# Performance work log

Measured on AMD Instinct MI355X. Metric: run time of the kernel, lower is better.

Reference implementation:

```python
import jax, jax.numpy as jnp
import numpy as np

K = 16          # self.nn_size
BALL2 = 0.2     # ball_size * 2, compared against squared L2 dists (faiss convention)

def _knn(q, db, k):
    # squared L2 pairwise distances (B,N,M) via ||q||^2 + ||db||^2 - 2 q.db
    d2 = (jnp.sum(q * q, -1)[..., None]
          + jnp.sum(db * db, -1)[..., None, :]
          - 2.0 * jnp.einsum('bnc,bmc->bnm', q, db))
    neg_d, idx = jax.lax.top_k(-d2, k)   # k smallest distances
    return -neg_d, idx                    # (B,N,K), (B,N,K)

def _cond_numbers(grouped, nball, B, N, C):
    # center by masked-ball mean, then singular values of (K,C) groups
    center = jnp.sum(grouped, axis=2, keepdims=True) / nball[..., None]
    centered = (grouped - center).reshape(-1, K, C)
    S = jnp.linalg.svd(centered, compute_uv=False)   # descending, (B*N, min(K,C))
    return (S[:, 0] / (S[:, -1] + S[:, 0])).reshape(B, N)

def setup_inputs() -> dict:
    key = jax.random.key(0)
    k1, k2 = jax.random.split(key)
    ref_points = jax.random.uniform(k1, (2, 8192, 3), dtype=jnp.float32)
    points = jax.random.uniform(k2, (2, 8192, 3), dtype=jnp.float32)
    return {"ref_points": ref_points, "points": points}

def reference(ref_points, points):
    B, N, C = ref_points.shape
    dist, idx = _knn(ref_points, ref_points, K)
    mask = dist < BALL2                                  # (B,N,K)
    nball = jnp.sum(mask.astype(ref_points.dtype), -1, keepdims=True)  # (B,N,1)

    gather = jax.vmap(lambda p, i: p[i])                 # (N,C),(N,K)->(N,K,C)
    grouped_ref = gather(ref_points, idx)                # (B,N,K,C)
    grouped_ref = jnp.where(mask[..., None], grouped_ref, 0.0)  # masked_fill_ (in-place, kept)
    ref_cond = _cond_numbers(grouped_ref, nball, B, N, C)

    grouped = gather(points, idx)                        # (B,N,K,C)
    # NOTE: original calls masked_fill (non-inplace) and DISCARDS the result -> no masking here
    cond = _cond_numbers(grouped, nball, B, N, C)

    # metric: MSE with mean reduction
    return jnp.mean((cond - ref_cond) ** 2)
```

## Files before the change

### kernel.cpp

```cpp
#include <hip/hip_runtime.h>

#define NPTS   8192
#define KNN    16
#define G      10
#define NCELLS 1000
#define CELLSZ 0.1f
#define BALL2f 0.2f
#define TRUNCM 0xFFFFE000u
#define IDXM   0x1FFFu
#define NBLK   256
#define FLTMAX 3.402823466e+38f

#define WS_ACC    0
#define WS_DONE   8
#define WS_STARTS 16
#define WS_RSORT  8032

__device__ __forceinline__ int clampg(int v) { return v < 0 ? 0 : (v > G - 1 ? G - 1 : v); }

__global__ __launch_bounds__(1024) void prep_kernel(
        const float* __restrict__ ref, int* __restrict__ gstarts,
        float4* __restrict__ rs, double* __restrict__ acc, int* __restrict__ done) {
    __shared__ int cnt[NCELLS];
    __shared__ int ssum[NCELLS + 1];
    __shared__ int wsum[16];
    const int b = blockIdx.x, t = threadIdx.x;
    const int w = t >> 6, lane = t & 63;
    if (b == 0 && t == 0) { acc[0] = 0.0; done[0] = 0; }
    if (t < NCELLS) cnt[t] = 0;
    __syncthreads();

    const float4* rb4 = reinterpret_cast<const float4*>(ref + (size_t)b * NPTS * 3) + t * 6;
    float4 A = rb4[0], B = rb4[1], C = rb4[2], D = rb4[3], E = rb4[4], F = rb4[5];
    float xs[8] = {A.x, A.w, B.z, C.y, D.x, D.w, E.z, F.y};
    float ys[8] = {A.y, B.x, B.w, C.z, D.y, E.x, E.w, F.z};
    float zs[8] = {A.z, B.y, C.x, C.w, D.z, E.y, F.x, F.w};
    int cells[8], slots[8];
    #pragma unroll
    for (int k = 0; k < 8; ++k) {
        int c = (clampg((int)(zs[k] * (float)G)) * G + clampg((int)(ys[k] * (float)G))) * G
              + clampg((int)(xs[k] * (float)G));
        cells[k] = c;
        slots[k] = atomicAdd(&cnt[c], 1);
    }
    __syncthreads();

    int v = (t < NCELLS) ? cnt[t] : 0;
    #pragma unroll
    for (int off = 1; off < 64; off <<= 1) {
        int u = __shfl_up(v, off, 64);
        if (lane >= off) v += u;
    }
    if (lane == 63) wsum[w] = v;
    __syncthreads();
    if (t == 0) {
        int run = 0;
        for (int i2 = 0; i2 < 16; ++i2) { int tv = wsum[i2]; wsum[i2] = run; run += tv; }
    }
    __syncthreads();
    if (t < NCELLS) ssum[t + 1] = v + wsum[w];
    if (t == 0) ssum[0] = 0;
    __syncthreads();
    if (t <= NCELLS) gstarts[b * (NCELLS + 1) + t] = ssum[t];

    #pragma unroll
    for (int k = 0; k < 8; ++k) {
        int pos = ssum[cells[k]] + slots[k];
        rs[(size_t)b * NPTS + pos] = make_float4(xs[k], ys[k], zs[k],
                                                 __uint_as_float((unsigned)(t * 8 + k)));
    }
}

__device__ __noinline__ double cond3(double xx, double xy, double xz,
                                     double yy, double yz, double zz) {
    double q  = (xx + yy + zz) * (1.0 / 3.0);
    double a  = xx - q, b = yy - q, c = zz - q;
    double p1 = xy * xy + xz * xz + yz * yz;
    double p2 = a * a + b * b + c * c + 2.0 * p1;
    if (p2 <= 0.0) return 0.5;
    double p   = sqrt(p2 * (1.0 / 6.0));
    double inv = 1.0 / p;
    double b00 = a * inv, b11 = b * inv, b22 = c * inv;
    double b01 = xy * inv, b02 = xz * inv, b12 = yz * inv;
    double detB = b00 * (b11 * b22 - b12 * b12)
                - b01 * (b01 * b22 - b12 * b02)
                + b02 * (b01 * b12 - b11 * b02);
    double r = 0.5 * detB;
    r = fmin(1.0, fmax(-1.0, r));
    double phi = acos(r) * (1.0 / 3.0);
    double l0 = q + 2.0 * p * cos(phi);
    double l2 = q + 2.0 * p * cos(phi + 2.0943951023931953);
    double s0 = sqrt(fmax(l0, 0.0));
    double s2 = sqrt(fmax(l2, 0.0));
    return s0 / (s0 + s2);
}

__global__ __launch_bounds__(1024) void cond_knn_kernel(
        const float* __restrict__ ref, const float* __restrict__ pts,
        const float4* __restrict__ rs, const int* __restrict__ gstarts,
        double* __restrict__ acc, int* __restrict__ done,
        float* __restrict__ out) {
    __shared__ unsigned sld[8][64][17];
    __shared__ int ss[NCELLS + 1];
    __shared__ unsigned cutp[64];
    __shared__ unsigned char doneA[64];
    __shared__ int flagS;

    const int tid  = threadIdx.x;
    const int w    = tid >> 6;
    const int lane = tid & 63;
    const int b     = blockIdx.x >> 7;
    const int qbase = (blockIdx.x & 127) << 6;
    const float4* rs4 = rs + (size_t)b * NPTS;

    for (int i = tid; i < NCELLS + 1; i += 1024)
        ss[i] = gstarts[b * (NCELLS + 1) + i];
    __syncthreads();

    float4 Q = rs4[qbase + lane];
    const float qx = Q.x, qy = Q.y, qz = Q.z;
    const int cx = clampg((int)(qx * (float)G));
    const int cy = clampg((int)(qy * (float)G));
    const int cz = clampg((int)(qz * (float)G));

    unsigned bq[KNN];
    #pragma unroll
    for (int k = 0; k < KNN; ++k) bq[k] = 0xFFFFFFFFu;

    auto ins1 = [&](unsigned vk, unsigned cutv) {
        unsigned cv = cutv < bq[15] ? cutv : bq[15];
        if (vk < cv) {
            bq[15] = vk;
            #pragma unroll
            for (int kk = 15; kk >= 1; --kk) {
                unsigned l2 = min(bq[kk - 1], bq[kk]);
                unsigned h2 = max(bq[kk - 1], bq[kk]);
                bq[kk - 1] = l2; bq[kk] = h2;
            }
        }
    };

    auto scanRange = [&](int s0, int s1, unsigned cutv) {
        int t2 = s0;
        for (; t2 + 4 <= s1; t2 += 4) {
            float4 P0 = rs4[t2 + 0];
            float4 P1 = rs4[t2 + 1];
            float4 P2 = rs4[t2 + 2];
            float4 P3 = rs4[t2 + 3];
            float dx0 = qx - P0.x, dy0 = qy - P0.y, dz0 = qz - P0.z;
            float dx1 = qx - P1.x, dy1 = qy - P1.y, dz1 = qz - P1.z;
            float dx2 = qx - P2.x, dy2 = qy - P2.y, dz2 = qz - P2.z;
            float dx3 = qx - P3.x, dy3 = qy - P3.y, dz3 = qz - P3.z;
            float d0 = fmaf(dx0, dx0, fmaf(dy0, dy0, dz0 * dz0));
            float d1 = fmaf(dx1, dx1, fmaf(dy1, dy1, dz1 * dz1));
            float d2 = fmaf(dx2, dx2, fmaf(dy2, dy2, dz2 * dz2));
            float d3 = fmaf(dx3, dx3, fmaf(dy3, dy3, dz3 * dz3));
            unsigned k0 = (__float_as_uint(d0) & TRUNCM) | __float_as_uint(P0.w);
            unsigned k1 = (__float_as_uint(d1) & TRUNCM) | __float_as_uint(P1.w);
            unsigned k2 = (__float_as_uint(d2) & TRUNCM) | __float_as_uint(P2.w);
            unsigned k3 = (__float_as_uint(d3) & TRUNCM) | __float_as_uint(P3.w);
            unsigned mn = min(min(k0, k1), min(k2, k3));
            unsigned cv = cutv < bq[15] ? cutv : bq[15];
            if (mn < cv) {
                ins1(k0, cutv); ins1(k1, cutv); ins1(k2, cutv); ins1(k3, cutv);
            }
        }
        for (; t2 < s1; ++t2) {
            float4 P = rs4[t2];
            float dx = qx - P.x, dy = qy - P.y, dz = qz - P.z;
            float d = fmaf(dx, dx, fmaf(dy, dy, dz * dz));
            ins1((__float_as_uint(d) & TRUNCM) | __float_as_uint(P.w), cutv);
        }
    };

    for (int it = w; it < 36; it += 16) {
        int q   = it & 3;
        int row = it >> 2;
        int dz = row / 3 - 1;
        int dy = row % 3 - 1;
        int ny = cy + dy, nz = cz + dz;
        if ((unsigned)ny > (unsigned)(G - 1) || (unsigned)nz > (unsigned)(G - 1)) continue;
        int x0 = cx - 1 < 0 ? 0 : cx - 1;
        int x1 = cx + 1 > G - 1 ? G - 1 : cx + 1;
        int c0 = (nz * G + ny) * G + x0;
        int s0 = ss[c0];
        int s1 = ss[c0 + (x1 - x0) + 1];
        int len = s1 - s0;
        int qs = s0 + ((len * q) >> 2);
        int qe = s0 + ((len * (q + 1)) >> 2);
        scanRange(qs, qe, 0xFFFFFFFFu);
    }

    for (int r = 2;; ++r) {
        #pragma unroll
        for (int rnd = 0; rnd < 4; ++rnd) {
            int s = 1 << rnd;
            int slot = w >> (rnd + 1);
            __syncthreads();
            if ((w & (2 * s - 1)) == s) {
                #pragma unroll
                for (int k = 0; k < KNN; ++k) sld[slot][lane][k] = bq[k];
            }
            __syncthreads();
            if ((w & (2 * s - 1)) == 0) {
                unsigned t[KNN];
                #pragma unroll
                for (int i = 0; i < KNN; ++i) t[i] = min(bq[i], sld[slot][lane][KNN - 1 - i]);
                #pragma unroll
                for (int s2 = 8; s2 >= 1; s2 >>= 1) {
                    #pragma unroll
                    for (int i = 0; i < KNN; ++i) {
                        if ((i & s2) == 0) {
                            unsigned l2 = min(t[i], t[i | s2]);
                            unsigned h2 = max(t[i], t[i | s2]);
                            t[i] = l2; t[i | s2] = h2;
                        }
                    }
                }
                #pragma unroll
                for (int k = 0; k < KNN; ++k) bq[k] = t[k];
            }
        }

        if (tid == 0) flagS = 0;
        __syncthreads();
        if (w == 0) {
            int rd = r - 1;
            float mx = FLTMAX;
            if (cx - rd > 0)     mx = fminf(mx, qx - (float)(cx - rd) * CELLSZ);
            if (cx + rd < G - 1) mx = fminf(mx, (float)(cx + rd + 1) * CELLSZ - qx);
            if (cy - rd > 0)     mx = fminf(mx, qy - (float)(cy - rd) * CELLSZ);
            if (cy + rd < G - 1) mx = fminf(mx, (float)(cy + rd + 1) * CELLSZ - qy);
            if (cz - rd > 0)     mx = fminf(mx, qz - (float)(cz - rd) * CELLSZ);
            if (cz + rd < G - 1) mx = fminf(mx, (float)(cz + rd + 1) * CELLSZ - qz);
            float d16t = __uint_as_float(bq[15] & TRUNCM);
            bool dn = d16t <= mx * mx * 0.998f;
            cutp[lane]  = bq[15];
            doneA[lane] = dn ? 1 : 0;
            if (__any(!dn) && lane == 0) flagS = 1;
        }
        __syncthreads();
        if (!flagS || r > G) break;

        if (w != 0) {
            #pragma unroll
            for (int k = 0; k < KNN; ++k) bq[k] = 0xFFFFFFFFu;
        }
        unsigned cut = cutp[lane];
        float cutub = __uint_as_float(cut | IDXM);
        bool active = !doneA[lane];
        int cc = 0;
        for (int dz = -r; dz <= r; ++dz)
        for (int dy = -r; dy <= r; ++dy)
        for (int dx = -r; dx <= r; ++dx) {
            int adx = dx < 0 ? -dx : dx, ady = dy < 0 ? -dy : dy, adz = dz < 0 ? -dz : dz;
            int m = adx > ady ? adx : ady; m = m > adz ? m : adz;
            if (m != r) continue;
            int myc = cc++;
            if ((myc & 15) != w) continue;
            if (!active) continue;
            int nx = cx + dx, ny = cy + dy, nz = cz + dz;
            if ((unsigned)nx > (unsigned)(G - 1) || (unsigned)ny > (unsigned)(G - 1) ||
                (unsigned)nz > (unsigned)(G - 1)) continue;
            float ex0 = (float)nx * CELLSZ;
            float ey0 = (float)ny * CELLSZ;
            float ez0 = (float)nz * CELLSZ;
            float ddx = fmaxf(0.f, fmaxf(ex0 - qx, qx - ex0 - CELLSZ));
            float ddy = fmaxf(0.f, fmaxf(ey0 - qy, qy - ey0 - CELLSZ));
            float ddz = fmaxf(0.f, fmaxf(ez0 - qz, qz - ez0 - CELLSZ));
            float d2min = fmaf(ddx, ddx, fmaf(ddy, ddy, ddz * ddz));
            if (d2min > cutub) continue;
            int cell = (nz * G + ny) * G + nx;
            scanRange(ss[cell], ss[cell + 1], cut);
        }
    }

    if (w != 0) return;

    const float* refb = ref + (size_t)b * NPTS * 3;
    const float* ptsb = pts + (size_t)b * NPTS * 3;
    float rx[KNN], ry[KNN], rz[KNN], px[KNN], py[KNN], pz[KNN];
    int mbits = 0;
    float sRx = 0.f, sRy = 0.f, sRz = 0.f, sPx = 0.f, sPy = 0.f, sPz = 0.f;
    #pragma unroll
    for (int k = 0; k < KNN; ++k) {
        int i = (int)(bq[k] & IDXM);
        float du = __uint_as_float(bq[k] & TRUNCM);
        rx[k] = refb[3 * i]; ry[k] = refb[3 * i + 1]; rz[k] = refb[3 * i + 2];
        px[k] = ptsb[3 * i]; py[k] = ptsb[3 * i + 1]; pz[k] = ptsb[3 * i + 2];
        if (du < BALL2f) {
            mbits |= (1 << k);
            sRx += rx[k]; sRy += ry[k]; sRz += rz[k];
        }
        sPx += px[k]; sPy += py[k]; sPz += pz[k];
    }
    int nb = __popc(mbits);
    double inb = 1.0 / (double)nb;
    double cRx = (double)sRx * inb, cRy = (double)sRy * inb, cRz = (double)sRz * inb;
    double cPx = (double)sPx * inb, cPy = (double)sPy * inb, cPz = (double)sPz * inb;

    double Rxx = 0, Rxy = 0, Rxz = 0, Ryy = 0, Ryz = 0, Rzz = 0;
    double Pxx = 0, Pxy = 0, Pxz = 0, Pyy = 0, Pyz = 0, Pzz = 0;
    #pragma unroll
    for (int k = 0; k < KNN; ++k) {
        bool m = (mbits >> k) & 1;
        double ax = (m ? (double)rx[k] : 0.0) - cRx;
        double ay = (m ? (double)ry[k] : 0.0) - cRy;
        double az = (m ? (double)rz[k] : 0.0) - cRz;
        Rxx += ax * ax; Rxy += ax * ay; Rxz += ax * az;
        Ryy += ay * ay; Ryz += ay * az; Rzz += az * az;
        double bx = (double)px[k] - cPx;
        double by = (double)py[k] - cPy;
        double bz = (double)pz[k] - cPz;
        Pxx += bx * bx; Pxy += bx * by; Pxz += bx * bz;
        Pyy += by * by; Pyz += by * bz; Pzz += bz * bz;
    }
    double condR = cond3(Rxx, Rxy, Rxz, Ryy, Ryz, Rzz);
    double condP = cond3(Pxx, Pxy, Pxz, Pyy, Pyz, Pzz);
    double t = condP - condR;
    t = t * t;

    #pragma unroll
    for (int off = 32; off > 0; off >>= 1) t += __shfl_down(t, off);
    if (lane == 0) {
        atomicAdd(acc, t);
        __threadfence();
        int prev = atomicAdd(done, 1);
        if (prev == NBLK - 1) {
            __threadfence();
            double total = atomicAdd(acc, 0.0);
            out[0] = (float)(total * (1.0 / 16384.0));
        }
    }
}

extern "C" void kernel_launch(void* const* d_in, const int* in_sizes, int n_in,
                              void* d_out, int out_size, void* d_ws, size_t ws_size,
                              hipStream_t stream) {
    const float* ref = (const float*)d_in[0];
    const float* pts = (const float*)d_in[1];
    char* ws = (char*)d_ws;
    double* acc   = (double*)(ws + WS_ACC);
    int* done     = (int*)(ws + WS_DONE);
    int* gstarts  = (int*)(ws + WS_STARTS);
    float4* rsort = (float4*)(ws + WS_RSORT);

    hipLaunchKernelGGL(prep_kernel,     dim3(2),    dim3(1024), 0, stream,
                       ref, gstarts, rsort, acc, done);
    hipLaunchKernelGGL(cond_knn_kernel, dim3(NBLK), dim3(1024), 0, stream,
                       ref, pts, rsort, gstarts, acc, done, (float*)d_out);
}
```

Measured before the change: 94.77 us.

## Use one wavefront per query block instead of sixteen cooperating waves

Each 64-query block now runs on a single wavefront that scans every neighbouring cell itself. This drops the shared-memory bitonic merges of per-wave top-16 lists, the block-wide barriers and the shared cut/done flags between search rings. The cost is less parallelism: 256 blocks of 64 threads put far fewer waves on the GPU, and each lane's serial scan grows about sixteenfold. Latency may therefore rise unless the removed sync and merge overhead was dominant.

```diff
diff --git a/kernel.cpp b/kernel.cpp
--- a/kernel.cpp
+++ b/kernel.cpp
@@ -95,25 +95,20 @@
     return s0 / (s0 + s2);
 }
 
-__global__ __launch_bounds__(1024) void cond_knn_kernel(
+__global__ __launch_bounds__(64) void cond_knn_kernel(
         const float* __restrict__ ref, const float* __restrict__ pts,
         const float4* __restrict__ rs, const int* __restrict__ gstarts,
         double* __restrict__ acc, int* __restrict__ done,
         float* __restrict__ out) {
-    __shared__ unsigned sld[8][64][17];
     __shared__ int ss[NCELLS + 1];
-    __shared__ unsigned cutp[64];
-    __shared__ unsigned char doneA[64];
-    __shared__ int flagS;
-
-    const int tid  = threadIdx.x;
-    const int w    = tid >> 6;
-    const int lane = tid & 63;
-    const int b     = blockIdx.x >> 7;
-    const int qbase = (blockIdx.x & 127) << 6;
+
+    const int lane = threadIdx.x;
+    const int blk  = blockIdx.x;
+    const int b     = blk >> 7;
+    const int qbase = (blk & 127) << 6;
     const float4* rs4 = rs + (size_t)b * NPTS;
 
-    for (int i = tid; i < NCELLS + 1; i += 1024)
+    for (int i = lane; i < NCELLS + 1; i += 64)
         ss[i] = gstarts[b * (NCELLS + 1) + i];
     __syncthreads();
 
@@ -127,9 +122,8 @@
     #pragma unroll
     for (int k = 0; k < KNN; ++k) bq[k] = 0xFFFFFFFFu;
 
-    auto ins1 = [&](unsigned vk, unsigned cutv) {
-        unsigned cv = cutv < bq[15] ? cutv : bq[15];
-        if (vk < cv) {
+    auto ins1 = [&](unsigned vk) {
+        if (vk < bq[15]) {
             bq[15] = vk;
             #pragma unroll
             for (int kk = 15; kk >= 1; --kk) {
@@ -140,7 +134,7 @@
         }
     };
 
-    auto scanRange = [&](int s0, int s1, unsigned cutv) {
+    auto scanRange = [&](int s0, int s1) {
         int t2 = s0;
         for (; t2 + 4 <= s1; t2 += 4) {
             float4 P0 = rs4[t2 + 0];
@@ -160,104 +154,58 @@
             unsigned k2 = (__float_as_uint(d2) & TRUNCM) | __float_as_uint(P2.w);
             unsigned k3 = (__float_as_uint(d3) & TRUNCM) | __float_as_uint(P3.w);
             unsigned mn = min(min(k0, k1), min(k2, k3));
-            unsigned cv = cutv < bq[15] ? cutv : bq[15];
-            if (mn < cv) {
-                ins1(k0, cutv); ins1(k1, cutv); ins1(k2, cutv); ins1(k3, cutv);
-            }
+            if (mn < bq[15]) { ins1(k0); ins1(k1); ins1(k2); ins1(k3); }
         }
         for (; t2 < s1; ++t2) {
             float4 P = rs4[t2];
             float dx = qx - P.x, dy = qy - P.y, dz = qz - P.z;
             float d = fmaf(dx, dx, fmaf(dy, dy, dz * dz));
-            ins1((__float_as_uint(d) & TRUNCM) | __float_as_uint(P.w), cutv);
+            ins1((__float_as_uint(d) & TRUNCM) | __float_as_uint(P.w));
         }
     };
 
-    for (int it = w; it < 36; it += 16) {
-        int q   = it & 3;
-        int row = it >> 2;
+    #pragma unroll 1
+    for (int row = 0; row < 9; ++row) {
         int dz = row / 3 - 1;
         int dy = row % 3 - 1;
         int ny = cy + dy, nz = cz + dz;
-        if ((unsigned)ny > (unsigned)(G - 1) || (unsigned)nz > (unsigned)(G - 1)) continue;
+        bool ok = (unsigned)ny <= (unsigned)(G - 1) && (unsigned)nz <= (unsigned)(G - 1);
         int x0 = cx - 1 < 0 ? 0 : cx - 1;
         int x1 = cx + 1 > G - 1 ? G - 1 : cx + 1;
         int c0 = (nz * G + ny) * G + x0;
-        int s0 = ss[c0];
-        int s1 = ss[c0 + (x1 - x0) + 1];
-        int len = s1 - s0;
-        int qs = s0 + ((len * q) >> 2);
-        int qe = s0 + ((len * (q + 1)) >> 2);
-        scanRange(qs, qe, 0xFFFFFFFFu);
-    }
-
-    for (int r = 2;; ++r) {
-        #pragma unroll
-        for (int rnd = 0; rnd < 4; ++rnd) {
-            int s = 1 << rnd;
-            int slot = w >> (rnd + 1);
-            __syncthreads();
-            if ((w & (2 * s - 1)) == s) {
-                #pragma unroll
-                for (int k = 0; k < KNN; ++k) sld[slot][lane][k] = bq[k];
-            }
-            __syncthreads();
-            if ((w & (2 * s - 1)) == 0) {
-                unsigned t[KNN];
-                #pragma unroll
-                for (int i = 0; i < KNN; ++i) t[i] = min(bq[i], sld[slot][lane][KNN - 1 - i]);
-                #pragma unroll
-                for (int s2 = 8; s2 >= 1; s2 >>= 1) {
-                    #pragma unroll
-                    for (int i = 0; i < KNN; ++i) {
-                        if ((i & s2) == 0) {
-                            unsigned l2 = min(t[i], t[i | s2]);
-                            unsigned h2 = max(t[i], t[i | s2]);
-                            t[i] = l2; t[i | s2] = h2;
-                        }
-                    }
-                }
-                #pragma unroll
-                for (int k = 0; k < KNN; ++k) bq[k] = t[k];
-            }
-        }
-
-        if (tid == 0) flagS = 0;
-        __syncthreads();
-        if (w == 0) {
-            int rd = r - 1;
-            float mx = FLTMAX;
-            if (cx - rd > 0)     mx = fminf(mx, qx - (float)(cx - rd) * CELLSZ);
-            if (cx + rd < G - 1) mx = fminf(mx, (float)(cx + rd + 1) * CELLSZ - qx);
-            if (cy - rd > 0)     mx = fminf(mx, qy - (float)(cy - rd) * CELLSZ);
-            if (cy + rd < G - 1) mx = fminf(mx, (float)(cy + rd + 1) * CELLSZ - qy);
-            if (cz - rd > 0)     mx = fminf(mx, qz - (float)(cz - rd) * CELLSZ);
-            if (cz + rd < G - 1) mx = fminf(mx, (float)(cz + rd + 1) * CELLSZ - qz);
-            float d16t = __uint_as_float(bq[15] & TRUNCM);
-            bool dn = d16t <= mx * mx * 0.998f;
-            cutp[lane]  = bq[15];
-            doneA[lane] = dn ? 1 : 0;
-            if (__any(!dn) && lane == 0) flagS = 1;
-        }
-        __syncthreads();
-        if (!flagS || r > G) break;
-
-        if (w != 0) {
-            #pragma unroll
-            for (int k = 0; k < KNN; ++k) bq[k] = 0xFFFFFFFFu;
-        }
-        unsigned cut = cutp[lane];
-        float cutub = __uint_as_float(cut | IDXM);
-        bool active = !doneA[lane];
-        int cc = 0;
+        int s0 = ok ? ss[c0] : 0;
+        int s1 = ok ? ss[c0 + (x1 - x0) + 1] : 0;
+        scanRange(s0, s1);
+    }
+
+    auto margin2 = [&](int rd) {
+        float mx = FLTMAX;
+        if (cx - rd > 0)     mx = fminf(mx, qx - (float)(cx - rd) * CELLSZ);
+        if (cx + rd < G - 1) mx = fminf(mx, (float)(cx + rd + 1) * CELLSZ - qx);
+        if (cy - rd > 0)     mx = fminf(mx, qy - (float)(cy - rd) * CELLSZ);
+        if (cy + rd < G - 1) mx = fminf(mx, (float)(cy + rd + 1) * CELLSZ - qy);
+        if (cz - rd > 0)     mx = fminf(mx, qz - (float)(cz - rd) * CELLSZ);
+        if (cz + rd < G - 1) mx = fminf(mx, (float)(cz + rd + 1) * CELLSZ - qz);
+        return mx * mx * 0.998f;
+    };
+
+    bool dn;
+    {
+        float d16t = __uint_as_float(bq[15] & TRUNCM);
+        dn = d16t <= margin2(1);
+    }
+    #pragma unroll 1
+    for (int r = 2; __any(!dn) && r <= G; ++r) {
+        bool active = !dn;
+        #pragma unroll 1
         for (int dz = -r; dz <= r; ++dz)
+        #pragma unroll 1
         for (int dy = -r; dy <= r; ++dy)
+        #pragma unroll 1
         for (int dx = -r; dx <= r; ++dx) {
             int adx = dx < 0 ? -dx : dx, ady = dy < 0 ? -dy : dy, adz = dz < 0 ? -dz : dz;
             int m = adx > ady ? adx : ady; m = m > adz ? m : adz;
             if (m != r) continue;
-            int myc = cc++;
-            if ((myc & 15) != w) continue;
             if (!active) continue;
             int nx = cx + dx, ny = cy + dy, nz = cz + dz;
             if ((unsigned)nx > (unsigned)(G - 1) || (unsigned)ny > (unsigned)(G - 1) ||
@@ -269,13 +217,14 @@
             float ddy = fmaxf(0.f, fmaxf(ey0 - qy, qy - ey0 - CELLSZ));
             float ddz = fmaxf(0.f, fmaxf(ez0 - qz, qz - ez0 - CELLSZ));
             float d2min = fmaf(ddx, ddx, fmaf(ddy, ddy, ddz * ddz));
+            float cutub = __uint_as_float(bq[15] | IDXM);
             if (d2min > cutub) continue;
             int cell = (nz * G + ny) * G + nx;
-            scanRange(ss[cell], ss[cell + 1], cut);
-        }
-    }
-
-    if (w != 0) return;
+            scanRange(ss[cell], ss[cell + 1]);
+        }
+        float d16t = __uint_as_float(bq[15] & TRUNCM);
+        dn = d16t <= margin2(r);
+    }
 
     const float* refb = ref + (size_t)b * NPTS * 3;
     const float* ptsb = pts + (size_t)b * NPTS * 3;
@@ -347,6 +296,6 @@
 
     hipLaunchKernelGGL(prep_kernel,     dim3(2),    dim3(1024), 0, stream,
                        ref, gstarts, rsort, acc, done);
-    hipLaunchKernelGGL(cond_knn_kernel, dim3(NBLK), dim3(1024), 0, stream,
+    hipLaunchKernelGGL(cond_knn_kernel, dim3(NBLK), dim3(64),   0, stream,
                        ref, pts, rsort, gstarts, acc, done, (float*)d_out);
 }
```

New measurement: 120.0 us. 26.7% more time.

## Split each query across two half-wavefronts and double block count

Applied to the files above, without the earlier changes.

Each block now handles 32 queries with 512 threads, and each query is processed by two lanes that scan disjoint halves of every cell range. The two partial top-16 lists are merged with a cross-half shuffle. This doubles the grid to 512 blocks so more of the GPU's compute units stay busy and per-lane scan length shrinks. The cost is an extra merge step and redundant work on the duplicated half-lanes during the epilogue.

```diff
diff --git a/kernel.cpp b/kernel.cpp
--- a/kernel.cpp
+++ b/kernel.cpp
@@ -8,7 +8,7 @@
 #define BALL2f 0.2f
 #define TRUNCM 0xFFFFE000u
 #define IDXM   0x1FFFu
-#define NBLK   256
+#define NBLK   512
 #define FLTMAX 3.402823466e+38f
 
 #define WS_ACC    0
@@ -95,29 +95,31 @@
     return s0 / (s0 + s2);
 }
 
-__global__ __launch_bounds__(1024) void cond_knn_kernel(
+__global__ __launch_bounds__(512, 4) void cond_knn_kernel(
         const float* __restrict__ ref, const float* __restrict__ pts,
         const float4* __restrict__ rs, const int* __restrict__ gstarts,
         double* __restrict__ acc, int* __restrict__ done,
         float* __restrict__ out) {
-    __shared__ unsigned sld[8][64][17];
     __shared__ int ss[NCELLS + 1];
-    __shared__ unsigned cutp[64];
-    __shared__ unsigned char doneA[64];
+    __shared__ unsigned sld[4][64][17];
+    __shared__ unsigned cutp[32];
+    __shared__ unsigned char doneA[32];
     __shared__ int flagS;
 
     const int tid  = threadIdx.x;
     const int w    = tid >> 6;
     const int lane = tid & 63;
-    const int b     = blockIdx.x >> 7;
-    const int qbase = (blockIdx.x & 127) << 6;
+    const int half = lane >> 5;
+    const int ql   = lane & 31;
+    const int b     = blockIdx.x >> 8;
+    const int qbase = (blockIdx.x & 255) << 5;
     const float4* rs4 = rs + (size_t)b * NPTS;
 
-    for (int i = tid; i < NCELLS + 1; i += 1024)
+    for (int i = tid; i < NCELLS + 1; i += 512)
         ss[i] = gstarts[b * (NCELLS + 1) + i];
     __syncthreads();
 
-    float4 Q = rs4[qbase + lane];
+    float4 Q = rs4[qbase + ql];
     const float qx = Q.x, qy = Q.y, qz = Q.z;
     const int cx = clampg((int)(qx * (float)G));
     const int cy = clampg((int)(qy * (float)G));
@@ -141,8 +143,11 @@
     };
 
     auto scanRange = [&](int s0, int s1, unsigned cutv) {
-        int t2 = s0;
-        for (; t2 + 4 <= s1; t2 += 4) {
+        int len = s1 - s0;
+        int a  = s0 + ((len * half) >> 1);
+        int e  = s0 + ((len * (half + 1)) >> 1);
+        int t2 = a;
+        for (; t2 + 4 <= e; t2 += 4) {
             float4 P0 = rs4[t2 + 0];
             float4 P1 = rs4[t2 + 1];
             float4 P2 = rs4[t2 + 2];
@@ -165,7 +170,7 @@
                 ins1(k0, cutv); ins1(k1, cutv); ins1(k2, cutv); ins1(k3, cutv);
             }
         }
-        for (; t2 < s1; ++t2) {
+        for (; t2 < e; ++t2) {
             float4 P = rs4[t2];
             float dx = qx - P.x, dy = qy - P.y, dz = qz - P.z;
             float d = fmaf(dx, dx, fmaf(dy, dy, dz * dz));
@@ -173,9 +178,28 @@
         }
     };
 
-    for (int it = w; it < 36; it += 16) {
-        int q   = it & 3;
-        int row = it >> 2;
+    auto merge16 = [&](const unsigned* inc) {
+        unsigned t[KNN];
+        #pragma unroll
+        for (int i = 0; i < KNN; ++i) t[i] = min(bq[i], inc[KNN - 1 - i]);
+        #pragma unroll
+        for (int s2 = 8; s2 >= 1; s2 >>= 1) {
+            #pragma unroll
+            for (int i = 0; i < KNN; ++i) {
+                if ((i & s2) == 0) {
+                    unsigned l2 = min(t[i], t[i | s2]);
+                    unsigned h2 = max(t[i], t[i | s2]);
+                    t[i] = l2; t[i | s2] = h2;
+                }
+            }
+        }
+        #pragma unroll
+        for (int k = 0; k < KNN; ++k) bq[k] = t[k];
+    };
+
+    for (int it = w; it < 18; it += 8) {
+        int row = it >> 1;
+        int sub = it & 1;
         int dz = row / 3 - 1;
         int dy = row % 3 - 1;
         int ny = cy + dy, nz = cz + dz;
@@ -183,17 +207,17 @@
         int x0 = cx - 1 < 0 ? 0 : cx - 1;
         int x1 = cx + 1 > G - 1 ? G - 1 : cx + 1;
         int c0 = (nz * G + ny) * G + x0;
-        int s0 = ss[c0];
-        int s1 = ss[c0 + (x1 - x0) + 1];
-        int len = s1 - s0;
-        int qs = s0 + ((len * q) >> 2);
-        int qe = s0 + ((len * (q + 1)) >> 2);
+        int rs0 = ss[c0];
+        int rs1 = ss[c0 + (x1 - x0) + 1];
+        int len = rs1 - rs0;
+        int qs = rs0 + ((len * sub) >> 1);
+        int qe = rs0 + ((len * (sub + 1)) >> 1);
         scanRange(qs, qe, 0xFFFFFFFFu);
     }
 
     for (int r = 2;; ++r) {
         #pragma unroll
-        for (int rnd = 0; rnd < 4; ++rnd) {
+        for (int rnd = 0; rnd < 3; ++rnd) {
             int s = 1 << rnd;
             int slot = w >> (rnd + 1);
             __syncthreads();
@@ -203,23 +227,17 @@
             }
             __syncthreads();
             if ((w & (2 * s - 1)) == 0) {
-                unsigned t[KNN];
+                unsigned inc[KNN];
                 #pragma unroll
-                for (int i = 0; i < KNN; ++i) t[i] = min(bq[i], sld[slot][lane][KNN - 1 - i]);
-                #pragma unroll
-                for (int s2 = 8; s2 >= 1; s2 >>= 1) {
-                    #pragma unroll
-                    for (int i = 0; i < KNN; ++i) {
-                        if ((i & s2) == 0) {
-                            unsigned l2 = min(t[i], t[i | s2]);
-                            unsigned h2 = max(t[i], t[i | s2]);
-                            t[i] = l2; t[i | s2] = h2;
-                        }
-                    }
-                }
-                #pragma unroll
-                for (int k = 0; k < KNN; ++k) bq[k] = t[k];
-            }
+                for (int k = 0; k < KNN; ++k) inc[k] = sld[slot][lane][k];
+                merge16(inc);
+            }
+        }
+        {
+            unsigned inc[KNN];
+            #pragma unroll
+            for (int k = 0; k < KNN; ++k) inc[k] = __shfl_xor(bq[k], 32, 64);
+            merge16(inc);
         }
 
         if (tid == 0) flagS = 0;
@@ -235,20 +253,19 @@
             if (cz + rd < G - 1) mx = fminf(mx, (float)(cz + rd + 1) * CELLSZ - qz);
             float d16t = __uint_as_float(bq[15] & TRUNCM);
             bool dn = d16t <= mx * mx * 0.998f;
-            cutp[lane]  = bq[15];
-            doneA[lane] = dn ? 1 : 0;
+            if (half == 0) { cutp[ql] = bq[15]; doneA[ql] = dn ? 1 : 0; }
             if (__any(!dn) && lane == 0) flagS = 1;
         }
         __syncthreads();
         if (!flagS || r > G) break;
 
-        if (w != 0) {
+        if (w != 0 || half == 1) {
             #pragma unroll
             for (int k = 0; k < KNN; ++k) bq[k] = 0xFFFFFFFFu;
         }
-        unsigned cut = cutp[lane];
+        unsigned cut = cutp[ql];
         float cutub = __uint_as_float(cut | IDXM);
-        bool active = !doneA[lane];
+        bool active = !doneA[ql];
         int cc = 0;
         for (int dz = -r; dz <= r; ++dz)
         for (int dy = -r; dy <= r; ++dy)
@@ -257,7 +274,7 @@
             int m = adx > ady ? adx : ady; m = m > adz ? m : adz;
             if (m != r) continue;
             int myc = cc++;
-            if ((myc & 15) != w) continue;
+            if ((myc & 7) != w) continue;
             if (!active) continue;
             int nx = cx + dx, ny = cy + dy, nz = cz + dz;
             if ((unsigned)nx > (unsigned)(G - 1) || (unsigned)ny > (unsigned)(G - 1) ||
@@ -319,6 +336,7 @@
     double condP = cond3(Pxx, Pxy, Pxz, Pyy, Pyz, Pzz);
     double t = condP - condR;
     t = t * t;
+    if (half == 1) t = 0.0;
 
     #pragma unroll
     for (int off = 32; off > 0; off >>= 1) t += __shfl_down(t, off);
@@ -347,6 +365,6 @@
 
     hipLaunchKernelGGL(prep_kernel,     dim3(2),    dim3(1024), 0, stream,
                        ref, gstarts, rsort, acc, done);
-    hipLaunchKernelGGL(cond_knn_kernel, dim3(NBLK), dim3(1024), 0, stream,
+    hipLaunchKernelGGL(cond_knn_kernel, dim3(NBLK), dim3(512),  0, stream,
                        ref, pts, rsort, gstarts, acc, done, (float*)d_out);
 }
```

After: 94.32 us. About the same (-0.5%).
